# Kernel tuning notes

Measured on AMD Instinct MI355X. Metric: run time of the kernel, lower is better.

Reference implementation:

```python
import jax, jax.numpy as jnp
import numpy as np

B, C, H, W = 64, 768, 26, 26
M = 32
K_ATT = 192
NUM_CLASSES = 200
EPS = 1e-12


def setup_inputs() -> dict:
    key = jax.random.key(0)
    k1, k2, k3, k4, k5 = jax.random.split(key, 5)
    return {
        "feature_maps": jax.random.normal(k1, (B, C, H, W), dtype=jnp.float32),
        "att_w": jax.random.normal(k2, (K_ATT, C), dtype=jnp.float32) * 0.02,
        "att_b": jax.random.normal(k3, (K_ATT,), dtype=jnp.float32) * 0.02,
        "fc_w": jax.random.normal(k4, (NUM_CLASSES, M * C), dtype=jnp.float32) * 0.02,
        "fc_b": jax.random.normal(k5, (NUM_CLASSES,), dtype=jnp.float32) * 0.02,
    }


def reference(feature_maps, att_w, att_b, fc_w, fc_b):
    b, c, h, w = feature_maps.shape
    # 1x1 attention conv + relu, keep first M maps
    att = jax.nn.relu(
        jnp.einsum("bchw,kc->bkhw", feature_maps, att_w)
        + att_b[None, :, None, None]
    )
    att_m = att[:, :M]  # [B, M, H, W]

    # BAP: the Python loop multiply+avgpool+concat is a single batched contraction
    fm = jnp.einsum("bmhw,bchw->bmc", att_m, feature_maps) / (h * w)
    # signed sqrt
    fm = jnp.sign(fm) * jnp.sqrt(jnp.abs(fm) + EPS)
    # L2 normalize over dims (1, 2), matching F.normalize(eps=1e-12)
    nrm = jnp.sqrt(jnp.sum(fm * fm, axis=(1, 2), keepdims=True))
    fm = fm / jnp.maximum(nrm, EPS)

    # fc 1x1 conv on [B, M*C, 1, 1] == dense GEMM; input scaled by 100
    p = (fm.reshape(b, M * c) * 100.0) @ fc_w.T + fc_b
    return p, fm, att_m
```

## Files before the change

kernel.cpp:

```cpp
#include <hip/hip_runtime.h>
#include <hip/hip_bf16.h>


typedef unsigned short u16;
typedef __bf16 bf16x8_t __attribute__((ext_vector_type(8)));
typedef float f32x4_t __attribute__((ext_vector_type(4)));
typedef unsigned int uint32x4 __attribute__((ext_vector_type(4)));
typedef unsigned int uint32x2 __attribute__((ext_vector_type(2)));

union Frag { uint32x4 u4; unsigned u[4]; u16 s[8]; bf16x8_t v; };
union BFU { __hip_bfloat16 h; u16 u; };

__device__ inline u16 f2b(float x) { BFU t; t.h = __float2bfloat16(x); return t.u; }

__device__ inline void load8_cvt(const float* p, Frag& f) {
    f32x4_t x0 = *(const f32x4_t*)(p);
    f32x4_t x1 = *(const f32x4_t*)(p + 4);
#pragma unroll
    for (int j = 0; j < 4; ++j) { f.s[j] = f2b(x0[j]); f.s[4 + j] = f2b(x1[j]); }
}

#define MFMA(a, b, c) __builtin_amdgcn_mfma_f32_16x16x32_bf16((a), (b), (c), 0, 0, 0)

__global__ __launch_bounds__(256) void k_cvt(
    const float* __restrict__ fm, u16* __restrict__ fmb16,
    float* __restrict__ p_sums)
{
    const int tid = blockIdx.x * 256 + threadIdx.x;
    if (blockIdx.x == 0 && threadIdx.x < 64) p_sums[threadIdx.x] = 0.f;
    const int cp  = tid % 176;
    const int row = tid / 176;
    u16* dst = fmb16 + (size_t)row * 704 + cp * 4;
    uint32x2 w;
    if (cp < 169) {
        f32x4_t x = *(const f32x4_t*)(fm + (size_t)row * 676 + cp * 4);
        w[0] = (unsigned)f2b(x[0]) | ((unsigned)f2b(x[1]) << 16);
        w[1] = (unsigned)f2b(x[2]) | ((unsigned)f2b(x[3]) << 16);
    } else {
        w[0] = 0u; w[1] = 0u;
    }
    *(uint32x2*)dst = w;
}

__global__ __launch_bounds__(256) void k_att(
    const u16* __restrict__ fmb16, const float* __restrict__ att_w,
    const float* __restrict__ att_b, float* __restrict__ att_out,
    __hip_bfloat16* __restrict__ att_pad)
{
    const int b  = blockIdx.y;
    const int p0 = blockIdx.x << 6;
    const int t  = threadIdx.x;
    const int wv = t >> 6, l = t & 63, q = l >> 4, ln = l & 15;

    __shared__ float red[32][64][4];

    f32x4_t acc[2][4];
#pragma unroll
    for (int i = 0; i < 2; ++i)
#pragma unroll
        for (int j = 0; j < 4; ++j) acc[i][j] = f32x4_t{0.f, 0.f, 0.f, 0.f};

    const int kb = wv * 192;
    const u16* Bbase = fmb16 + (size_t)b * 768 * 704 + p0;

#pragma unroll
    for (int it = 0; it < 6; ++it) {
        const int k0 = kb + it * 32;
        Frag a0, a1, bf[4];
        load8_cvt(att_w + (size_t)ln * 768 + k0 + q * 8, a0);
        load8_cvt(att_w + (size_t)(16 + ln) * 768 + k0 + q * 8, a1);
        const u16* bp = Bbase + (size_t)(k0 + q * 8) * 704 + ln;
#pragma unroll
        for (int pc = 0; pc < 4; ++pc)
#pragma unroll
            for (int j = 0; j < 8; ++j)
                bf[pc].s[j] = bp[(size_t)j * 704 + pc * 16];
#pragma unroll
        for (int pc = 0; pc < 4; ++pc) {
            acc[0][pc] = MFMA(a0.v, bf[pc].v, acc[0][pc]);
            acc[1][pc] = MFMA(a1.v, bf[pc].v, acc[1][pc]);
        }
    }

#pragma unroll
    for (int mh = 0; mh < 2; ++mh)
#pragma unroll
        for (int pc = 0; pc < 4; ++pc)
#pragma unroll
            for (int r = 0; r < 4; ++r)
                red[mh * 16 + q * 4 + r][pc * 16 + ln][wv] = acc[mh][pc][r];
    __syncthreads();

    const int m  = t >> 3;
    const int pg = (t & 7) << 3;
    const float bias = att_b[m];
#pragma unroll
    for (int g = 0; g < 2; ++g) {
        const int pl = pg + g * 4;
        const int p  = p0 + pl;
        f32x4_t v;
        u16 h[4];
#pragma unroll
        for (int j = 0; j < 4; ++j) {
            f32x4_t r4 = *(const f32x4_t*)&red[m][pl + j][0];
            float x = r4[0] + r4[1] + r4[2] + r4[3] + bias;
            x = x > 0.f ? x : 0.f;
            v[j] = x;
            h[j] = (p + j < 676) ? f2b(x) : (u16)0;
        }
        if (p <= 672)
            *(f32x4_t*)(att_out + (size_t)(b * 32 + m) * 676 + p) = v;
        uint32x2 w;
        w[0] = (unsigned)h[0] | ((unsigned)h[1] << 16);
        w[1] = (unsigned)h[2] | ((unsigned)h[3] << 16);
        *(uint32x2*)((u16*)att_pad + (size_t)(b * 32 + m) * 704 + p) = w;
    }
}

__global__ __launch_bounds__(256) void k_pool(
    const u16* __restrict__ fmb16, const u16* __restrict__ att_pad,
    float* __restrict__ pooled, float* __restrict__ p_sums)
{
    const int b  = blockIdx.y;
    const int n0 = blockIdx.x << 5;
    const int t  = threadIdx.x;
    const int wv = t >> 6, l = t & 63, q = l >> 4, ln = l & 15;

    __shared__ float red[32][32][4];
    __shared__ float rs[4];

    const u16* Ab = att_pad + (size_t)b * 32 * 704;
    const u16* B0 = fmb16 + (size_t)(b * 768 + n0 + ln) * 704;
    const u16* B1 = fmb16 + (size_t)(b * 768 + n0 + 16 + ln) * 704;

    f32x4_t acc[2][2] = {{{0.f,0.f,0.f,0.f},{0.f,0.f,0.f,0.f}},
                         {{0.f,0.f,0.f,0.f},{0.f,0.f,0.f,0.f}}};

    for (int it = wv; it < 22; it += 4) {
        const int k = it * 32 + q * 8;
        Frag a0, a1, b0, b1;
        a0.u4 = *(const uint32x4*)(Ab + (size_t)ln * 704 + k);
        a1.u4 = *(const uint32x4*)(Ab + (size_t)(16 + ln) * 704 + k);
        b0.u4 = *(const uint32x4*)(B0 + k);
        b1.u4 = *(const uint32x4*)(B1 + k);
        acc[0][0] = MFMA(a0.v, b0.v, acc[0][0]);
        acc[0][1] = MFMA(a0.v, b1.v, acc[0][1]);
        acc[1][0] = MFMA(a1.v, b0.v, acc[1][0]);
        acc[1][1] = MFMA(a1.v, b1.v, acc[1][1]);
    }

#pragma unroll
    for (int mh = 0; mh < 2; ++mh)
#pragma unroll
        for (int ch = 0; ch < 2; ++ch)
#pragma unroll
            for (int r = 0; r < 4; ++r)
                red[mh * 16 + q * 4 + r][ch * 16 + ln][wv] = acc[mh][ch][r];
    __syncthreads();

    const float sc = 1.0f / 676.0f;
    const int m = t >> 3, c0 = (t & 7) << 2;
    float ls = 0.f;
#pragma unroll
    for (int j = 0; j < 4; ++j) {
        const int cl = c0 + j;
        f32x4_t v4 = *(const f32x4_t*)&red[m][cl][0];
        float v = (v4[0] + v4[1] + v4[2] + v4[3]) * sc;
        pooled[(size_t)(b * 32 + m) * 768 + n0 + cl] = v;
        ls += fabsf(v);
    }
    for (int off = 32; off > 0; off >>= 1) ls += __shfl_down(ls, off);
    if (l == 0) rs[wv] = ls;
    __syncthreads();
    if (t == 0) atomicAdd(p_sums + b, rs[0] + rs[1] + rs[2] + rs[3]);
}

__global__ __launch_bounds__(256) void k_norm(
    const float* __restrict__ pooled, const float* __restrict__ p_sums,
    float* __restrict__ fm_out, u16* __restrict__ fmn16)
{
    const int b = blockIdx.x;
    const size_t base = (size_t)b * 24576 + (size_t)blockIdx.y * 2048;
    const float tot = p_sums[b] + 24576.f * 1e-12f;
    const float inv = 1.f / fmaxf(sqrtf(tot), 1e-12f);
    const int t = threadIdx.x;
#pragma unroll
    for (int i = 0; i < 8; ++i) {
        const size_t idx = base + i * 256 + t;
        float x = pooled[idx];
        float v = (x == 0.f) ? 0.f : copysignf(sqrtf(fabsf(x) + 1e-12f), x);
        float o = v * inv;
        fm_out[idx] = o;
        fmn16[idx]  = f2b(o);
    }
}

__global__ __launch_bounds__(256) void k_fc(
    const u16* __restrict__ fmn16, const float* __restrict__ fc_w,
    float* __restrict__ p_part)
{
    const int ntile = blockIdx.x;
    const int slab  = blockIdx.y;
    const int t = threadIdx.x;
    const int wv = t >> 6, l = t & 63, q = l >> 4, ln = l & 15;
    const int n = ntile * 16 + ln;
    const int kbase = slab * 512;

    const u16*   Ab = fmn16 + (size_t)(wv * 16 + ln) * 24576 + kbase + q * 8;
    const float* Bb = fc_w + (size_t)n * 24576 + kbase + q * 8;
    const bool nok = n < 200;

    f32x4_t acc = {0.f, 0.f, 0.f, 0.f};
#pragma unroll
    for (int kk = 0; kk < 512; kk += 32) {
        Frag af, bf2;
        af.u4 = *(const uint32x4*)(Ab + kk);
        if (nok) load8_cvt(Bb + kk, bf2);
        else { bf2.u[0] = 0u; bf2.u[1] = 0u; bf2.u[2] = 0u; bf2.u[3] = 0u; }
        acc = MFMA(af.v, bf2.v, acc);
    }
#pragma unroll
    for (int r = 0; r < 4; ++r) {
        const int bb = wv * 16 + q * 4 + r;
        p_part[(size_t)(slab * 64 + bb) * 208 + ntile * 16 + ln] = acc[r];
    }
}

__global__ __launch_bounds__(256) void k_fin(
    const float* __restrict__ p_part, const float* __restrict__ fc_b,
    float* __restrict__ p_out)
{
    const int tid = blockIdx.x * 256 + threadIdx.x;
    const int b = tid / 200, n = tid - b * 200;
    float s = 0.f;
#pragma unroll
    for (int sl = 0; sl < 48; ++sl) s += p_part[(size_t)(sl * 64 + b) * 208 + n];
    p_out[tid] = s * 100.f + fc_b[n];
}

extern "C" void kernel_launch(void* const* d_in, const int* in_sizes, int n_in,
                              void* d_out, int out_size, void* d_ws, size_t ws_size,
                              hipStream_t stream)
{
    const float* fm    = (const float*)d_in[0];
    const float* att_w = (const float*)d_in[1];
    const float* att_b = (const float*)d_in[2];
    const float* fc_w  = (const float*)d_in[3];
    const float* fc_b  = (const float*)d_in[4];

    float* out     = (float*)d_out;
    float* p_out   = out;
    float* fm_out  = out + 12800;
    float* att_out = out + 12800 + 64 * 32 * 768;

    char* ws = (char*)d_ws;
    u16* fmb16 = (u16*)ws;
    __hip_bfloat16* att_pad = (__hip_bfloat16*)(ws + 69206016);
    float* p_part = (float*)(ws + 69206016);
    float* pooled = (float*)(ws + 69206016 + 2883584);
    u16*   fmn16  = (u16*)(ws + 69206016 + 2883584 + 6291456);
    float* p_sums = (float*)(ws + 69206016 + 2883584 + 6291456 + 3145728);

    k_cvt <<<dim3(33792), 256, 0, stream>>>(fm, fmb16, p_sums);
    k_att <<<dim3(11, 64), 256, 0, stream>>>(fmb16, att_w, att_b, att_out, att_pad);
    k_pool<<<dim3(24, 64), 256, 0, stream>>>(fmb16, (const u16*)att_pad, pooled, p_sums);
    k_norm<<<dim3(64, 12), 256, 0, stream>>>(pooled, p_sums, fm_out, fmn16);
    k_fc  <<<dim3(13, 48), 256, 0, stream>>>(fmn16, fc_w, p_part);
    k_fin <<<dim3(50),     256, 0, stream>>>(p_part, fc_b, p_out);
}
```

Baseline: 279.1 us.

## Fuse fp32-to-bf16 conversion into the attention GEMM kernel via an LDS tile

Removes the separate conversion kernel. The attention kernel now loads fp32 feature maps directly, converts them to bf16, and stages them in a shared-memory tile. It also writes the padded bf16 copy for the later pooling kernel. Each wave now owns a 16-column slice over the full K range instead of splitting K across waves, which removes the LDS cross-wave reduction. The cost is that the K loop now has block-level syncs, and each block does more serial global loading with lower MFMA parallelism per wave.

```diff
diff --git a/kernel.cpp b/kernel.cpp
--- a/kernel.cpp
+++ b/kernel.cpp
@@ -22,98 +22,74 @@
 
 #define MFMA(a, b, c) __builtin_amdgcn_mfma_f32_16x16x32_bf16((a), (b), (c), 0, 0, 0)
 
-__global__ __launch_bounds__(256) void k_cvt(
-    const float* __restrict__ fm, u16* __restrict__ fmb16,
+__global__ __launch_bounds__(256) void k_att(
+    const float* __restrict__ fm, const float* __restrict__ att_w,
+    const float* __restrict__ att_b, float* __restrict__ att_out,
+    __hip_bfloat16* __restrict__ att_pad, u16* __restrict__ fmb16,
     float* __restrict__ p_sums)
-{
-    const int tid = blockIdx.x * 256 + threadIdx.x;
-    if (blockIdx.x == 0 && threadIdx.x < 64) p_sums[threadIdx.x] = 0.f;
-    const int cp  = tid % 176;
-    const int row = tid / 176;
-    u16* dst = fmb16 + (size_t)row * 704 + cp * 4;
-    uint32x2 w;
-    if (cp < 169) {
-        f32x4_t x = *(const f32x4_t*)(fm + (size_t)row * 676 + cp * 4);
-        w[0] = (unsigned)f2b(x[0]) | ((unsigned)f2b(x[1]) << 16);
-        w[1] = (unsigned)f2b(x[2]) | ((unsigned)f2b(x[3]) << 16);
-    } else {
-        w[0] = 0u; w[1] = 0u;
-    }
-    *(uint32x2*)dst = w;
-}
-
-__global__ __launch_bounds__(256) void k_att(
-    const u16* __restrict__ fmb16, const float* __restrict__ att_w,
-    const float* __restrict__ att_b, float* __restrict__ att_out,
-    __hip_bfloat16* __restrict__ att_pad)
 {
     const int b  = blockIdx.y;
     const int p0 = blockIdx.x << 6;
     const int t  = threadIdx.x;
     const int wv = t >> 6, l = t & 63, q = l >> 4, ln = l & 15;
 
-    __shared__ float red[32][64][4];
-
-    f32x4_t acc[2][4];
-#pragma unroll
-    for (int i = 0; i < 2; ++i)
-#pragma unroll
-        for (int j = 0; j < 4; ++j) acc[i][j] = f32x4_t{0.f, 0.f, 0.f, 0.f};
-
-    const int kb = wv * 192;
-    const u16* Bbase = fmb16 + (size_t)b * 768 * 704 + p0;
-
-#pragma unroll
-    for (int it = 0; it < 6; ++it) {
-        const int k0 = kb + it * 32;
-        Frag a0, a1, bf[4];
-        load8_cvt(att_w + (size_t)ln * 768 + k0 + q * 8, a0);
-        load8_cvt(att_w + (size_t)(16 + ln) * 768 + k0 + q * 8, a1);
-        const u16* bp = Bbase + (size_t)(k0 + q * 8) * 704 + ln;
-#pragma unroll
-        for (int pc = 0; pc < 4; ++pc)
+    if (blockIdx.x == 0 && b == 0 && t < 64) p_sums[t] = 0.f;
+
+    __shared__ u16 tile[128 * 66];
+
+    f32x4_t acc[2] = {{0.f,0.f,0.f,0.f},{0.f,0.f,0.f,0.f}};
+
+    const int  sr   = t >> 3;
+    const int  sc8  = (t & 7) << 3;
+    const bool edge = (p0 + sc8 + 7) >= 676;
+
+    for (int k0 = 0; k0 < 768; k0 += 128) {
+        if (k0) __syncthreads();
+#pragma unroll
+        for (int s = 0; s < 4; ++s) {
+            const int r = sr + 32 * s;
+            const float* src = fm + (size_t)(b * 768 + k0 + r) * 676 + p0 + sc8;
+            Frag val;
+            if (!edge) {
+                load8_cvt(src, val);
+            } else {
+#pragma unroll
+                for (int i = 0; i < 8; ++i)
+                    val.s[i] = (p0 + sc8 + i < 676) ? f2b(src[i]) : (u16)0;
+            }
+            unsigned* dst = (unsigned*)&tile[r * 66 + sc8];
+            dst[0]=val.u[0]; dst[1]=val.u[1]; dst[2]=val.u[2]; dst[3]=val.u[3];
+            *(uint32x4*)(fmb16 + (size_t)(b * 768 + k0 + r) * 704 + p0 + sc8) = val.u4;
+        }
+        __syncthreads();
+
+#pragma unroll
+        for (int ks = 0; ks < 4; ++ks) {
+            const int kk = k0 + ks * 32;
+            Frag a0, a1, bfr;
+            load8_cvt(att_w + (size_t)ln * 768 + kk + q * 8, a0);
+            load8_cvt(att_w + (size_t)(16 + ln) * 768 + kk + q * 8, a1);
+            const int rb = ks * 32 + q * 8;
 #pragma unroll
             for (int j = 0; j < 8; ++j)
-                bf[pc].s[j] = bp[(size_t)j * 704 + pc * 16];
-#pragma unroll
-        for (int pc = 0; pc < 4; ++pc) {
-            acc[0][pc] = MFMA(a0.v, bf[pc].v, acc[0][pc]);
-            acc[1][pc] = MFMA(a1.v, bf[pc].v, acc[1][pc]);
+                bfr.s[j] = tile[(rb + j) * 66 + wv * 16 + ln];
+            acc[0] = MFMA(a0.v, bfr.v, acc[0]);
+            acc[1] = MFMA(a1.v, bfr.v, acc[1]);
         }
     }
 
-#pragma unroll
-    for (int mh = 0; mh < 2; ++mh)
-#pragma unroll
-        for (int pc = 0; pc < 4; ++pc)
-#pragma unroll
-            for (int r = 0; r < 4; ++r)
-                red[mh * 16 + q * 4 + r][pc * 16 + ln][wv] = acc[mh][pc][r];
-    __syncthreads();
-
-    const int m  = t >> 3;
-    const int pg = (t & 7) << 3;
-    const float bias = att_b[m];
-#pragma unroll
-    for (int g = 0; g < 2; ++g) {
-        const int pl = pg + g * 4;
-        const int p  = p0 + pl;
-        f32x4_t v;
-        u16 h[4];
-#pragma unroll
-        for (int j = 0; j < 4; ++j) {
-            f32x4_t r4 = *(const f32x4_t*)&red[m][pl + j][0];
-            float x = r4[0] + r4[1] + r4[2] + r4[3] + bias;
+    const int  p   = p0 + wv * 16 + ln;
+    const bool pok = p < 676;
+#pragma unroll
+    for (int mh = 0; mh < 2; ++mh) {
+#pragma unroll
+        for (int r = 0; r < 4; ++r) {
+            const int m = mh * 16 + q * 4 + r;
+            float x = acc[mh][r] + att_b[m];
             x = x > 0.f ? x : 0.f;
-            v[j] = x;
-            h[j] = (p + j < 676) ? f2b(x) : (u16)0;
+            ((u16*)att_pad)[(size_t)(b * 32 + m) * 704 + p] = pok ? f2b(x) : (u16)0;
+            if (pok) att_out[(size_t)(b * 32 + m) * 676 + p] = x;
         }
-        if (p <= 672)
-            *(f32x4_t*)(att_out + (size_t)(b * 32 + m) * 676 + p) = v;
-        uint32x2 w;
-        w[0] = (unsigned)h[0] | ((unsigned)h[1] << 16);
-        w[1] = (unsigned)h[2] | ((unsigned)h[3] << 16);
-        *(uint32x2*)((u16*)att_pad + (size_t)(b * 32 + m) * 704 + p) = w;
     }
 }
 
@@ -261,8 +237,7 @@
     u16*   fmn16  = (u16*)(ws + 69206016 + 2883584 + 6291456);
     float* p_sums = (float*)(ws + 69206016 + 2883584 + 6291456 + 3145728);
 
-    k_cvt <<<dim3(33792), 256, 0, stream>>>(fm, fmb16, p_sums);
-    k_att <<<dim3(11, 64), 256, 0, stream>>>(fmb16, att_w, att_b, att_out, att_pad);
+    k_att <<<dim3(11, 64), 256, 0, stream>>>(fm, att_w, att_b, att_out, att_pad, fmb16, p_sums);
     k_pool<<<dim3(24, 64), 256, 0, stream>>>(fmb16, (const u16*)att_pad, pooled, p_sums);
     k_norm<<<dim3(64, 12), 256, 0, stream>>>(pooled, p_sums, fm_out, fmn16);
     k_fc  <<<dim3(13, 48), 256, 0, stream>>>(fmn16, fc_w, p_part);
```

New measurement: 294.0 us. 5.3% more time.
